# Optimization experiments

Measured on AMD Instinct MI355X. Metric: run time of the kernel, lower is better.

The kernel has to match this reference:

```python
import jax, jax.numpy as jnp
import numpy as np

EPS = 1e-05
KARCHER_STEPS = 1
B, N = 32768, 32


def _sym_fn(x, fn):
    # Apply fn to eigenvalues of symmetric x: V diag(fn(w)) V^T
    w, v = jnp.linalg.eigh(x)
    return jnp.einsum('...ij,...j,...kj->...ik', v, fn(w), v)


def _logm(x):
    return _sym_fn(x, jnp.log)


def _expm(x):
    return _sym_fn(x, jnp.exp)


def _mat_pow(x, p):
    return _sym_fn(x, lambda w: w ** p)


def _sqrt_and_isqrt(x):
    # One eigh shared between the +1/2 and -1/2 powers of the mean
    w, v = jnp.linalg.eigh(x)
    s = jnp.sqrt(w)
    sqrt = jnp.einsum('...ij,...j,...kj->...ik', v, s, v)
    isqrt = jnp.einsum('...ij,...j,...kj->...ik', v, 1.0 / s, v)
    return sqrt, isqrt


def karcher_flow(x, steps):
    # Karcher (Frechet) mean under AIRM, initialized at the arithmetic mean
    mean = x.mean(axis=0)
    for _ in range(steps):
        m_s, m_is = _sqrt_and_isqrt(mean)
        t = _logm(m_is @ x @ m_is).mean(axis=0)  # tangent-space mean at `mean`
        mean = m_s @ _expm(t) @ m_s
    return mean


def airm_distance(x, mean):
    _, m_is = _sqrt_and_isqrt(mean)
    l = _logm(m_is @ x @ m_is)
    return jnp.sqrt(jnp.sum(l * l, axis=(-2, -1)))


def setup_inputs() -> dict:
    key = jax.random.key(0)
    a = jax.random.normal(key, (B, N, N), dtype=jnp.float32)
    # Well-conditioned SPD batch: Wishart/N + 0.1 I
    x = a @ a.swapaxes(-1, -2) / N + 0.1 * jnp.eye(N, dtype=jnp.float32)
    scale = jnp.ones((1,), dtype=jnp.float32)
    return {"x": x, "scale": scale}


def reference(x, scale):
    # Training-mode batch statistics (computed under no_grad in the original)
    mean = jax.lax.stop_gradient(karcher_flow(x, KARCHER_STEPS))
    d = airm_distance(jax.lax.stop_gradient(x), mean)
    std = jax.lax.stop_gradient(jnp.sqrt(jnp.mean(d ** 2, axis=0)))
    # riemannian_batch_norm: parallel transport to identity, then matrix power
    _, m_is = _sqrt_and_isqrt(mean)
    xt = m_is @ x @ m_is
    p = scale[0] / (std + EPS)
    return _mat_pow(xt, p)
```

## Files before the change

### kernel.cpp

```cpp
#include <hip/hip_runtime.h>
#include <math.h>

#define BATCH 32768
#define MELEM 1024
#define NSWEEP_BATCH 7
#define NSWEEP_PREP 8
#define MPW 4
#define NW (BATCH / (2 * MPW))
#define NBLK (NW / 4)
#define G0 512
#define EPSF 1e-5f

#define WS_M0    0
#define WS_MS0   1024
#define WS_MIS0  2048
#define WS_T     3072
#define WS_MIS1  4096
#define WS_P     5120
#define WS_D2    5184

#define STG_F 2368
#define GT_H 1152
#define GT_LD 36


__device__ __forceinline__ float colnorm(const float (&col)[32]) {
    float a0 = 0, a1 = 0, a2 = 0, a3 = 0;
#pragma unroll
    for (int k = 0; k < 32; k += 4) {
        a0 = fmaf(col[k], col[k], a0);
        a1 = fmaf(col[k + 1], col[k + 1], a1);
        a2 = fmaf(col[k + 2], col[k + 2], a2);
        a3 = fmaf(col[k + 3], col[k + 3], a3);
    }
    return (a0 + a1) + (a2 + a3);
}

__device__ __forceinline__ void onesided_sweeps(float (&col)[32], float &nrm, int nsweeps) {
    for (int sw = 0; sw < nsweeps; ++sw) {
        for (int m = 1; m < 32; ++m) {
            float t[32];
            float npart = __shfl_xor(nrm, m);
            float a0 = 0, a1 = 0, a2 = 0, a3 = 0;
#pragma unroll
            for (int k = 0; k < 32; k += 4) {
                t[k] = __shfl_xor(col[k], m);
                t[k + 1] = __shfl_xor(col[k + 1], m);
                t[k + 2] = __shfl_xor(col[k + 2], m);
                t[k + 3] = __shfl_xor(col[k + 3], m);
                a0 = fmaf(col[k], t[k], a0);
                a1 = fmaf(col[k + 1], t[k + 1], a1);
                a2 = fmaf(col[k + 2], t[k + 2], a2);
                a3 = fmaf(col[k + 3], t[k + 3], a3);
            }
            float apq = (a0 + a1) + (a2 + a3);
            if (apq * apq > 1e-14f * nrm * npart) {
                float tau = (npart - nrm) * 0.5f / apq;
                float tt = copysignf(1.f / (fabsf(tau) + sqrtf(fmaf(tau, tau, 1.f))), tau);
                float cc = rsqrtf(fmaf(tt, tt, 1.f));
                float ss = tt * cc;
                nrm = cc * cc * nrm - 2.f * cc * ss * apq + ss * ss * npart;
#pragma unroll
                for (int k = 0; k < 32; ++k) col[k] = fmaf(cc, col[k], -ss * t[k]);
            }
        }
    }
}

__device__ __forceinline__ void sxs_col(const float* Xh, const float* Sl,
                                        const float (&sreg)[32], float (&z)[32]) {
    float u[32];
#pragma unroll
    for (int i = 0; i < 32; ++i) {
        float a0 = 0, a1 = 0, a2 = 0, a3 = 0;
#pragma unroll
        for (int k = 0; k < 32; k += 4) {
            const float4 xr = *reinterpret_cast<const float4*>(&Xh[i * 32 + k]);
            a0 = fmaf(xr.x, sreg[k], a0);
            a1 = fmaf(xr.y, sreg[k + 1], a1);
            a2 = fmaf(xr.z, sreg[k + 2], a2);
            a3 = fmaf(xr.w, sreg[k + 3], a3);
        }
        u[i] = (a0 + a1) + (a2 + a3);
    }
#pragma unroll
    for (int i = 0; i < 32; ++i) {
        float a0 = 0, a1 = 0, a2 = 0, a3 = 0;
#pragma unroll
        for (int k = 0; k < 32; k += 4) {
            const float4 sr = *reinterpret_cast<const float4*>(&Sl[i * 32 + k]);
            a0 = fmaf(sr.x, u[k], a0);
            a1 = fmaf(sr.y, u[k + 1], a1);
            a2 = fmaf(sr.z, u[k + 2], a2);
            a3 = fmaf(sr.w, u[k + 3], a3);
        }
        z[i] = (a0 + a1) + (a2 + a3);
    }
}

__device__ __forceinline__ void stage_gt(float* Gth, float* wth, int c,
                                         const float (&col)[32], float wtv) {
#pragma unroll
    for (int k = 0; k < 32; k += 4)
        *reinterpret_cast<float4*>(&Gth[c * GT_LD + k]) =
            make_float4(col[k], col[k + 1], col[k + 2], col[k + 3]);
    wth[c] = wtv;
}

__device__ __forceinline__ void recon_accum(const float* Gth, const float* wth, int c,
                                            float (&acc)[32]) {
    for (int j = 0; j < 32; ++j) {
        float coef = wth[j] * Gth[j * GT_LD + c];
#pragma unroll
        for (int k = 0; k < 32; k += 4) {
            const float4 g = *reinterpret_cast<const float4*>(&Gth[j * GT_LD + k]);
            acc[k] = fmaf(coef, g.x, acc[k]);
            acc[k + 1] = fmaf(coef, g.y, acc[k + 1]);
            acc[k + 2] = fmaf(coef, g.z, acc[k + 2]);
            acc[k + 3] = fmaf(coef, g.w, acc[k + 3]);
        }
    }
}

__device__ __forceinline__ float half_reduce(float v) {
    v += __shfl_xor(v, 1); v += __shfl_xor(v, 2); v += __shfl_xor(v, 4);
    v += __shfl_xor(v, 8); v += __shfl_xor(v, 16);
    return v;
}


__global__ __launch_bounds__(256) void k_mean_partial(const float* __restrict__ x,
                                                      float* __restrict__ part) {
    int g = blockIdx.x, tid = threadIdx.x;
    const float* base = x + (size_t)g * 64 * MELEM;
    float a0 = 0, a1 = 0, a2 = 0, a3 = 0;
    for (int b = 0; b < 64; ++b) {
        const float* m = base + b * MELEM;
        a0 += m[tid]; a1 += m[tid + 256]; a2 += m[tid + 512]; a3 += m[tid + 768];
    }
    float* o = part + (size_t)g * MELEM;
    o[tid] = a0; o[tid + 256] = a1; o[tid + 512] = a2; o[tid + 768] = a3;
}

__global__ __launch_bounds__(256) void k_reduce(const float* __restrict__ part,
                                                float* __restrict__ dst, int G, float scale) {
    __shared__ float sm[256];
    int e = blockIdx.x, tid = threadIdx.x;
    float acc = 0.f;
    for (int g = tid; g < G; g += 256) acc += part[(size_t)g * MELEM + e];
    sm[tid] = acc;
    __syncthreads();
    for (int off = 128; off > 0; off >>= 1) {
        if (tid < off) sm[tid] += sm[tid + off];
        __syncthreads();
    }
    if (tid == 0) dst[e] = sm[0] * scale;
}


__global__ __launch_bounds__(64) void k_prep0(float* __restrict__ ws) {
    __shared__ alignas(16) float stage[STG_F];
    const int lane = threadIdx.x, h = lane >> 5, c = lane & 31;
    float col[32];
#pragma unroll
    for (int i = 0; i < 32; ++i) col[i] = ws[WS_M0 + i * 32 + c];
    float nrm = colnorm(col);
    onesided_sweeps(col, nrm, NSWEEP_PREP);
    nrm = colnorm(col);
    float* Gth = &stage[h * GT_H];
    float* wth = &stage[2304 + h * 32];
    float lnn = logf(nrm);
    stage_gt(Gth, wth, c, col, expf(-0.75f * lnn));
    float acc[32];
#pragma unroll
    for (int i = 0; i < 32; ++i) acc[i] = 0.f;
    recon_accum(Gth, wth, c, acc);
    if (h == 0) {
#pragma unroll
        for (int i = 0; i < 32; ++i) ws[WS_MS0 + i * 32 + c] = acc[i];
    }
    wth[c] = expf(-1.25f * lnn);
#pragma unroll
    for (int i = 0; i < 32; ++i) acc[i] = 0.f;
    recon_accum(Gth, wth, c, acc);
    if (h == 0) {
#pragma unroll
        for (int i = 0; i < 32; ++i) ws[WS_MIS0 + i * 32 + c] = acc[i];
    }
}


__global__ __launch_bounds__(256, 3) void k_pass_logm(const float* __restrict__ x,
                                                      const float* __restrict__ ws,
                                                      float* __restrict__ part) {
    __shared__ alignas(16) float Sl[1024];
    __shared__ alignas(16) float stage[4][STG_F];
    const int tid = threadIdx.x;
    const int wid = tid >> 6, lane = tid & 63, h = lane >> 5, c = lane & 31;
    for (int e = tid; e < 1024; e += 256) Sl[e] = ws[WS_MIS0 + e];
    __syncthreads();
    float* Xw = &stage[wid][0];
    const float* Xh = Xw + h * 1024;
    float* Gth = &stage[wid][h * GT_H];
    float* wth = &stage[wid][2304 + h * 32];
    float Lacc[32];
#pragma unroll
    for (int i = 0; i < 32; ++i) Lacc[i] = 0.f;
    const int gw = blockIdx.x * 4 + wid;
    for (int mm = 0; mm < MPW; ++mm) {
        const size_t pairBase = ((size_t)(gw * MPW + mm)) * 2048;
        const float4* gx = reinterpret_cast<const float4*>(x + pairBase);
        float4* X4 = reinterpret_cast<float4*>(Xw);
#pragma unroll
        for (int ch = 0; ch < 8; ++ch) X4[ch * 64 + lane] = gx[ch * 64 + lane];
        float sreg[32];
#pragma unroll
        for (int k = 0; k < 32; ++k) sreg[k] = Sl[k * 32 + c];
        float col[32];
        sxs_col(Xh, Sl, sreg, col);
        float nrm = colnorm(col);
        onesided_sweeps(col, nrm, NSWEEP_BATCH);
        nrm = colnorm(col);
        float wtv = 0.5f * logf(nrm) / nrm;
        stage_gt(Gth, wth, c, col, wtv);
        recon_accum(Gth, wth, c, Lacc);
    }
#pragma unroll
    for (int i = 0; i < 32; ++i) {
        float v = Lacc[i] + __shfl_xor(Lacc[i], 32);
        if (h == 0) part[(size_t)gw * MELEM + i * 32 + c] = v;
    }
}


__global__ __launch_bounds__(64) void k_prep1(float* __restrict__ ws) {
    __shared__ alignas(16) float Sl[1024];
    __shared__ alignas(16) float stage[STG_F];
    const int lane = threadIdx.x, h = lane >> 5, c = lane & 31;
    float* Xw = &stage[0];
    const float* Xh = Xw + h * 1024;
    float* Gth = &stage[h * GT_H];
    float* wth = &stage[2304 + h * 32];

    float col[32];
#pragma unroll
    for (int i = 0; i < 32; ++i) col[i] = ws[WS_T + i * 32 + c];
    float nrm = colnorm(col);
    float fro2 = half_reduce(nrm);
    float alpha = sqrtf(fro2) + 1.0f;
#pragma unroll
    for (int i = 0; i < 32; ++i) col[i] += (i == c) ? alpha : 0.f;
    nrm = colnorm(col);
    onesided_sweeps(col, nrm, NSWEEP_PREP);
    nrm = colnorm(col);
    float nu = sqrtf(nrm);
    stage_gt(Gth, wth, c, col, expf(nu - alpha) / nrm);
    float acc[32];
#pragma unroll
    for (int i = 0; i < 32; ++i) acc[i] = 0.f;
    recon_accum(Gth, wth, c, acc);
#pragma unroll
    for (int i = 0; i < 32; ++i) Xw[h * 1024 + i * 32 + c] = acc[i];
    for (int e = lane; e < 1024; e += 64) Sl[e] = ws[WS_MS0 + e];
    __syncthreads();
    float sreg[32];
#pragma unroll
    for (int k = 0; k < 32; ++k) sreg[k] = Sl[k * 32 + c];
    sxs_col(Xh, Sl, sreg, col);
    nrm = colnorm(col);
    onesided_sweeps(col, nrm, NSWEEP_PREP);
    nrm = colnorm(col);
    stage_gt(Gth, wth, c, col, expf(-1.25f * logf(nrm)));
#pragma unroll
    for (int i = 0; i < 32; ++i) acc[i] = 0.f;
    recon_accum(Gth, wth, c, acc);
    if (h == 0) {
#pragma unroll
        for (int i = 0; i < 32; ++i) ws[WS_MIS1 + i * 32 + c] = acc[i];
    }
}


__global__ __launch_bounds__(256, 3) void k_pass_dist(const float* __restrict__ x,
                                                      float* __restrict__ ws,
                                                      float* __restrict__ outG) {
    __shared__ alignas(16) float Sl[1024];
    __shared__ alignas(16) float stage[4][STG_F];
    const int tid = threadIdx.x;
    const int wid = tid >> 6, lane = tid & 63, h = lane >> 5, c = lane & 31;
    for (int e = tid; e < 1024; e += 256) Sl[e] = ws[WS_MIS1 + e];
    __syncthreads();
    float* Xw = &stage[wid][0];
    const float* Xh = Xw + h * 1024;
    const int gw = blockIdx.x * 4 + wid;
    float d2acc = 0.f;
    for (int mm = 0; mm < MPW; ++mm) {
        const size_t pairBase = ((size_t)(gw * MPW + mm)) * 2048;
        const float4* gx = reinterpret_cast<const float4*>(x + pairBase);
        float4* X4 = reinterpret_cast<float4*>(Xw);
#pragma unroll
        for (int ch = 0; ch < 8; ++ch) X4[ch * 64 + lane] = gx[ch * 64 + lane];
        float sreg[32];
#pragma unroll
        for (int k = 0; k < 32; ++k) sreg[k] = Sl[k * 32 + c];
        float col[32];
        sxs_col(Xh, Sl, sreg, col);
        float nrm = colnorm(col);
        onesided_sweeps(col, nrm, NSWEEP_BATCH);
        nrm = colnorm(col);
#pragma unroll
        for (int i = 0; i < 32; ++i) outG[pairBase + h * 1024 + i * 32 + c] = col[i];
        float lg = 0.5f * logf(nrm);
        float l2 = lg * lg;
#pragma unroll
        for (int m = 1; m <= 32; m <<= 1) l2 += __shfl_xor(l2, m);
        d2acc += l2;
    }
    if (lane == 0) ws[WS_D2 + gw] = d2acc;
}

__global__ __launch_bounds__(256) void k_finish_p(float* __restrict__ ws,
                                                  const float* __restrict__ scale) {
    __shared__ float sm[256];
    int tid = threadIdx.x;
    float acc = 0.f;
    for (int g = tid; g < NW; g += 256) acc += ws[WS_D2 + g];
    sm[tid] = acc;
    __syncthreads();
    for (int off = 128; off > 0; off >>= 1) {
        if (tid < off) sm[tid] += sm[tid + off];
        __syncthreads();
    }
    if (tid == 0) {
        float sd = sqrtf(sm[0] / (float)BATCH);
        ws[WS_P] = scale[0] / (sd + EPSF);
    }
}


__global__ __launch_bounds__(256, 4) void k_out_recon(float* __restrict__ outG,
                                                      const float* __restrict__ ws) {
    __shared__ alignas(16) float stage[4][STG_F];
    const int tid = threadIdx.x;
    const int wid = tid >> 6, lane = tid & 63, h = lane >> 5, c = lane & 31;
    float* Gth = &stage[wid][h * GT_H];
    float* wth = &stage[wid][2304 + h * 32];
    const float p = ws[WS_P];
    const float ex = 0.5f * p - 1.0f;
    const int gw = blockIdx.x * 4 + wid;
    for (int mm = 0; mm < MPW; ++mm) {
        const size_t pairBase = ((size_t)(gw * MPW + mm)) * 2048;
        float col[32];
#pragma unroll
        for (int i = 0; i < 32; ++i) col[i] = outG[pairBase + h * 1024 + i * 32 + c];
        float nrm = colnorm(col);
        stage_gt(Gth, wth, c, col, expf(ex * logf(nrm)));
        float acc[32];
#pragma unroll
        for (int i = 0; i < 32; ++i) acc[i] = 0.f;
        recon_accum(Gth, wth, c, acc);
#pragma unroll
        for (int i = 0; i < 32; ++i) outG[pairBase + h * 1024 + i * 32 + c] = acc[i];
    }
}


extern "C" void kernel_launch(void* const* d_in, const int* in_sizes, int n_in,
                              void* d_out, int out_size, void* d_ws, size_t ws_size,
                              hipStream_t stream) {
    const float* x = (const float*)d_in[0];
    const float* scale = (const float*)d_in[1];
    float* out = (float*)d_out;
    float* ws = (float*)d_ws;

    k_mean_partial<<<G0, 256, 0, stream>>>(x, out);
    k_reduce<<<MELEM, 256, 0, stream>>>(out, ws + WS_M0, G0, 1.0f / (float)BATCH);
    k_prep0<<<1, 64, 0, stream>>>(ws);
    k_pass_logm<<<NBLK, 256, 0, stream>>>(x, ws, out);
    k_reduce<<<MELEM, 256, 0, stream>>>(out, ws + WS_T, NW, 1.0f / (float)BATCH);
    k_prep1<<<1, 64, 0, stream>>>(ws);
    k_pass_dist<<<NBLK, 256, 0, stream>>>(x, ws, out);
    k_finish_p<<<1, 256, 0, stream>>>(ws, scale);
    k_out_recon<<<NBLK, 256, 0, stream>>>(out, ws);
}
```

Measured before the change: 3.570 ms.

## Raise occupancy by shrinking LDS staging and moving logm reduction out of pass

Per-column weights are folded into the padded column of the staged eigenvector tile, which removes the separate weight array and shrinks per-wave shared memory. The distance pass gets a smaller staging buffer, and the logm and dist passes are relaunched with four blocks per CU instead of three. The logm pass stops accumulating per-wave partial sums in registers; it writes every reconstructed log matrix to global memory, and a separate partial-sum kernel plus a simple per-element reduce compute the mean. This frees registers and LDS but adds a large global write and read of the full batch, and the new 4-block reduce is serial per element.

Result: slower. 4.458 ms (+24.9%).

```diff
diff --git a/kernel.cpp b/kernel.cpp
--- a/kernel.cpp
+++ b/kernel.cpp
@@ -18,10 +18,12 @@
 #define WS_MIS1  4096
 #define WS_P     5120
 #define WS_D2    5184
-
-#define STG_F 2368
+#define WS_PART2 16384
+#define WS_NEED_BIG ((WS_PART2 + G0 * MELEM) * sizeof(float))
+
+#define GT_LD 36
 #define GT_H 1152
-#define GT_LD 36
+#define STG_F 2304
 
 
 __device__ __forceinline__ float colnorm(const float (&col)[32]) {
@@ -68,7 +70,10 @@
 }
 
 __device__ __forceinline__ void sxs_col(const float* Xh, const float* Sl,
-                                        const float (&sreg)[32], float (&z)[32]) {
+                                        int c, float (&z)[32]) {
+    float sreg[32];
+#pragma unroll
+    for (int k = 0; k < 32; ++k) sreg[k] = Sl[k * 32 + c];
     float u[32];
 #pragma unroll
     for (int i = 0; i < 32; ++i) {
@@ -98,19 +103,17 @@
     }
 }
 
-__device__ __forceinline__ void stage_gt(float* Gth, float* wth, int c,
-                                         const float (&col)[32], float wtv) {
+__device__ __forceinline__ void stage_gt(float* Gth, int c, const float (&col)[32], float wtv) {
 #pragma unroll
     for (int k = 0; k < 32; k += 4)
         *reinterpret_cast<float4*>(&Gth[c * GT_LD + k]) =
             make_float4(col[k], col[k + 1], col[k + 2], col[k + 3]);
-    wth[c] = wtv;
-}
-
-__device__ __forceinline__ void recon_accum(const float* Gth, const float* wth, int c,
-                                            float (&acc)[32]) {
+    Gth[c * GT_LD + 32] = wtv;
+}
+
+__device__ __forceinline__ void recon_accum(const float* Gth, int c, float (&acc)[32]) {
     for (int j = 0; j < 32; ++j) {
-        float coef = wth[j] * Gth[j * GT_LD + c];
+        float coef = Gth[j * GT_LD + 32] * Gth[j * GT_LD + c];
 #pragma unroll
         for (int k = 0; k < 32; k += 4) {
             const float4 g = *reinterpret_cast<const float4*>(&Gth[j * GT_LD + k]);
@@ -142,19 +145,13 @@
     o[tid] = a0; o[tid + 256] = a1; o[tid + 512] = a2; o[tid + 768] = a3;
 }
 
-__global__ __launch_bounds__(256) void k_reduce(const float* __restrict__ part,
-                                                float* __restrict__ dst, int G, float scale) {
-    __shared__ float sm[256];
-    int e = blockIdx.x, tid = threadIdx.x;
+__global__ __launch_bounds__(256) void k_reduce_small(const float* __restrict__ src,
+                                                      float* __restrict__ dst,
+                                                      int G, float scale) {
+    int e = blockIdx.x * 256 + threadIdx.x;
     float acc = 0.f;
-    for (int g = tid; g < G; g += 256) acc += part[(size_t)g * MELEM + e];
-    sm[tid] = acc;
-    __syncthreads();
-    for (int off = 128; off > 0; off >>= 1) {
-        if (tid < off) sm[tid] += sm[tid + off];
-        __syncthreads();
-    }
-    if (tid == 0) dst[e] = sm[0] * scale;
+    for (int g = 0; g < G; ++g) acc += src[(size_t)g * MELEM + e];
+    dst[e] = acc * scale;
 }
 
 
@@ -168,21 +165,20 @@
     onesided_sweeps(col, nrm, NSWEEP_PREP);
     nrm = colnorm(col);
     float* Gth = &stage[h * GT_H];
-    float* wth = &stage[2304 + h * 32];
     float lnn = logf(nrm);
-    stage_gt(Gth, wth, c, col, expf(-0.75f * lnn));
+    stage_gt(Gth, c, col, expf(-0.75f * lnn));
     float acc[32];
 #pragma unroll
     for (int i = 0; i < 32; ++i) acc[i] = 0.f;
-    recon_accum(Gth, wth, c, acc);
+    recon_accum(Gth, c, acc);
     if (h == 0) {
 #pragma unroll
         for (int i = 0; i < 32; ++i) ws[WS_MS0 + i * 32 + c] = acc[i];
     }
-    wth[c] = expf(-1.25f * lnn);
+    Gth[c * GT_LD + 32] = expf(-1.25f * lnn);
 #pragma unroll
     for (int i = 0; i < 32; ++i) acc[i] = 0.f;
-    recon_accum(Gth, wth, c, acc);
+    recon_accum(Gth, c, acc);
     if (h == 0) {
 #pragma unroll
         for (int i = 0; i < 32; ++i) ws[WS_MIS0 + i * 32 + c] = acc[i];
@@ -190,9 +186,9 @@
 }
 
 
-__global__ __launch_bounds__(256, 3) void k_pass_logm(const float* __restrict__ x,
+__global__ __launch_bounds__(256, 4) void k_pass_logm(const float* __restrict__ x,
                                                       const float* __restrict__ ws,
-                                                      float* __restrict__ part) {
+                                                      float* __restrict__ Lout) {
     __shared__ alignas(16) float Sl[1024];
     __shared__ alignas(16) float stage[4][STG_F];
     const int tid = threadIdx.x;
@@ -202,10 +198,6 @@
     float* Xw = &stage[wid][0];
     const float* Xh = Xw + h * 1024;
     float* Gth = &stage[wid][h * GT_H];
-    float* wth = &stage[wid][2304 + h * 32];
-    float Lacc[32];
-#pragma unroll
-    for (int i = 0; i < 32; ++i) Lacc[i] = 0.f;
     const int gw = blockIdx.x * 4 + wid;
     for (int mm = 0; mm < MPW; ++mm) {
         const size_t pairBase = ((size_t)(gw * MPW + mm)) * 2048;
@@ -213,22 +205,18 @@
         float4* X4 = reinterpret_cast<float4*>(Xw);
 #pragma unroll
         for (int ch = 0; ch < 8; ++ch) X4[ch * 64 + lane] = gx[ch * 64 + lane];
-        float sreg[32];
-#pragma unroll
-        for (int k = 0; k < 32; ++k) sreg[k] = Sl[k * 32 + c];
         float col[32];
-        sxs_col(Xh, Sl, sreg, col);
+        sxs_col(Xh, Sl, c, col);
         float nrm = colnorm(col);
         onesided_sweeps(col, nrm, NSWEEP_BATCH);
         nrm = colnorm(col);
-        float wtv = 0.5f * logf(nrm) / nrm;
-        stage_gt(Gth, wth, c, col, wtv);
-        recon_accum(Gth, wth, c, Lacc);
-    }
-#pragma unroll
-    for (int i = 0; i < 32; ++i) {
-        float v = Lacc[i] + __shfl_xor(Lacc[i], 32);
-        if (h == 0) part[(size_t)gw * MELEM + i * 32 + c] = v;
+        stage_gt(Gth, c, col, 0.5f * logf(nrm) / nrm);
+        float acc[32];
+#pragma unroll
+        for (int i = 0; i < 32; ++i) acc[i] = 0.f;
+        recon_accum(Gth, c, acc);
+#pragma unroll
+        for (int i = 0; i < 32; ++i) Lout[pairBase + h * 1024 + i * 32 + c] = acc[i];
     }
 }
 
@@ -240,7 +228,6 @@
     float* Xw = &stage[0];
     const float* Xh = Xw + h * 1024;
     float* Gth = &stage[h * GT_H];
-    float* wth = &stage[2304 + h * 32];
 
     float col[32];
 #pragma unroll
@@ -254,26 +241,23 @@
     onesided_sweeps(col, nrm, NSWEEP_PREP);
     nrm = colnorm(col);
     float nu = sqrtf(nrm);
-    stage_gt(Gth, wth, c, col, expf(nu - alpha) / nrm);
+    stage_gt(Gth, c, col, expf(nu - alpha) / nrm);
     float acc[32];
 #pragma unroll
     for (int i = 0; i < 32; ++i) acc[i] = 0.f;
-    recon_accum(Gth, wth, c, acc);
+    recon_accum(Gth, c, acc);
 #pragma unroll
     for (int i = 0; i < 32; ++i) Xw[h * 1024 + i * 32 + c] = acc[i];
     for (int e = lane; e < 1024; e += 64) Sl[e] = ws[WS_MS0 + e];
     __syncthreads();
-    float sreg[32];
-#pragma unroll
-    for (int k = 0; k < 32; ++k) sreg[k] = Sl[k * 32 + c];
-    sxs_col(Xh, Sl, sreg, col);
+    sxs_col(Xh, Sl, c, col);
     nrm = colnorm(col);
     onesided_sweeps(col, nrm, NSWEEP_PREP);
     nrm = colnorm(col);
-    stage_gt(Gth, wth, c, col, expf(-1.25f * logf(nrm)));
+    stage_gt(Gth, c, col, expf(-1.25f * logf(nrm)));
 #pragma unroll
     for (int i = 0; i < 32; ++i) acc[i] = 0.f;
-    recon_accum(Gth, wth, c, acc);
+    recon_accum(Gth, c, acc);
     if (h == 0) {
 #pragma unroll
         for (int i = 0; i < 32; ++i) ws[WS_MIS1 + i * 32 + c] = acc[i];
@@ -281,16 +265,16 @@
 }
 
 
-__global__ __launch_bounds__(256, 3) void k_pass_dist(const float* __restrict__ x,
+__global__ __launch_bounds__(256, 4) void k_pass_dist(const float* __restrict__ x,
                                                       float* __restrict__ ws,
                                                       float* __restrict__ outG) {
     __shared__ alignas(16) float Sl[1024];
-    __shared__ alignas(16) float stage[4][STG_F];
+    __shared__ alignas(16) float stageX[4][2048];
     const int tid = threadIdx.x;
     const int wid = tid >> 6, lane = tid & 63, h = lane >> 5, c = lane & 31;
     for (int e = tid; e < 1024; e += 256) Sl[e] = ws[WS_MIS1 + e];
     __syncthreads();
-    float* Xw = &stage[wid][0];
+    float* Xw = &stageX[wid][0];
     const float* Xh = Xw + h * 1024;
     const int gw = blockIdx.x * 4 + wid;
     float d2acc = 0.f;
@@ -300,11 +284,8 @@
         float4* X4 = reinterpret_cast<float4*>(Xw);
 #pragma unroll
         for (int ch = 0; ch < 8; ++ch) X4[ch * 64 + lane] = gx[ch * 64 + lane];
-        float sreg[32];
-#pragma unroll
-        for (int k = 0; k < 32; ++k) sreg[k] = Sl[k * 32 + c];
         float col[32];
-        sxs_col(Xh, Sl, sreg, col);
+        sxs_col(Xh, Sl, c, col);
         float nrm = colnorm(col);
         onesided_sweeps(col, nrm, NSWEEP_BATCH);
         nrm = colnorm(col);
@@ -344,7 +325,6 @@
     const int tid = threadIdx.x;
     const int wid = tid >> 6, lane = tid & 63, h = lane >> 5, c = lane & 31;
     float* Gth = &stage[wid][h * GT_H];
-    float* wth = &stage[wid][2304 + h * 32];
     const float p = ws[WS_P];
     const float ex = 0.5f * p - 1.0f;
     const int gw = blockIdx.x * 4 + wid;
@@ -354,11 +334,11 @@
 #pragma unroll
         for (int i = 0; i < 32; ++i) col[i] = outG[pairBase + h * 1024 + i * 32 + c];
         float nrm = colnorm(col);
-        stage_gt(Gth, wth, c, col, expf(ex * logf(nrm)));
+        stage_gt(Gth, c, col, expf(ex * logf(nrm)));
         float acc[32];
 #pragma unroll
         for (int i = 0; i < 32; ++i) acc[i] = 0.f;
-        recon_accum(Gth, wth, c, acc);
+        recon_accum(Gth, c, acc);
 #pragma unroll
         for (int i = 0; i < 32; ++i) outG[pairBase + h * 1024 + i * 32 + c] = acc[i];
     }
@@ -372,12 +352,18 @@
     const float* scale = (const float*)d_in[1];
     float* out = (float*)d_out;
     float* ws = (float*)d_ws;
+    const bool big = ws_size >= WS_NEED_BIG;
 
     k_mean_partial<<<G0, 256, 0, stream>>>(x, out);
-    k_reduce<<<MELEM, 256, 0, stream>>>(out, ws + WS_M0, G0, 1.0f / (float)BATCH);
+    k_reduce_small<<<4, 256, 0, stream>>>(out, ws + WS_M0, G0, 1.0f / (float)BATCH);
     k_prep0<<<1, 64, 0, stream>>>(ws);
     k_pass_logm<<<NBLK, 256, 0, stream>>>(x, ws, out);
-    k_reduce<<<MELEM, 256, 0, stream>>>(out, ws + WS_T, NW, 1.0f / (float)BATCH);
+    if (big) {
+        k_mean_partial<<<G0, 256, 0, stream>>>(out, ws + WS_PART2);
+        k_reduce_small<<<4, 256, 0, stream>>>(ws + WS_PART2, ws + WS_T, G0, 1.0f / (float)BATCH);
+    } else {
+        k_reduce_small<<<4, 256, 0, stream>>>(out, ws + WS_T, BATCH, 1.0f / (float)BATCH);
+    }
     k_prep1<<<1, 64, 0, stream>>>(ws);
     k_pass_dist<<<NBLK, 256, 0, stream>>>(x, ws, out);
     k_finish_p<<<1, 256, 0, stream>>>(ws, scale);
```
